# Kernel optimization log

Hardware: AMD Instinct MI355X
Metric: run time of the kernel (lower is better)

The kernel has to match this reference:

```python
import jax, jax.numpy as jnp
import numpy as np

N_USERS = 100000
N_ITEMS = 50000
N_NODES = N_USERS + N_ITEMS
NNZ = 3200000
DIM = 64
N_LAYERS = 3
BATCH = 8192


def setup_inputs() -> dict:
    key = jax.random.key(0)
    ks = jax.random.split(key, 8)
    user_emb = jax.random.normal(ks[0], (N_USERS, DIM), dtype=jnp.float32) * 0.1
    item_emb0 = jnp.zeros((N_ITEMS, DIM), dtype=jnp.float32)
    edge_val = jax.random.uniform(ks[1], (NNZ,), dtype=jnp.float32)
    W = jax.random.normal(ks[2], (DIM, DIM), dtype=jnp.float32) / np.sqrt(DIM)
    b = jax.random.normal(ks[3], (DIM,), dtype=jnp.float32) * 0.01
    edge_src = jax.random.randint(ks[4], (NNZ,), 0, N_NODES, dtype=jnp.int32)
    edge_dst = jax.random.randint(ks[5], (NNZ,), 0, N_NODES, dtype=jnp.int32)
    users = jax.random.randint(ks[6], (BATCH,), 0, N_USERS, dtype=jnp.int32)
    items = jax.random.randint(ks[7], (BATCH,), 0, N_ITEMS, dtype=jnp.int32)
    return {"user_emb": user_emb, "item_emb0": item_emb0, "edge_val": edge_val,
            "W": W, "b": b, "edge_src": edge_src, "edge_dst": edge_dst,
            "users": users, "items": items}


def _spmm(edge_src, edge_dst, edge_val, x):
    # y[dst] += val * x[src]  -- COO SpMM via segment_sum
    msgs = edge_val[:, None] * x[edge_src]          # [nnz, d]
    return jax.ops.segment_sum(msgs, edge_dst, num_segments=N_NODES)


def reference(user_emb, item_emb0, edge_val, W, b, edge_src, edge_dst, users, items):
    all_emb = jnp.concatenate([user_emb, item_emb0], axis=0)  # [N, d]
    embs = [all_emb]
    for _ in range(N_LAYERS):
        all_emb = _spmm(edge_src, edge_dst, edge_val, all_emb)
        embs.append(all_emb)
    # per-layer: transform item slice, keep ORIGINAL user_emb for user slice
    new_embs = []
    for e in embs:
        item_t = e[N_USERS:] @ W.T + b                 # Linear(d, d)
        new_embs.append(jnp.concatenate([user_emb, item_t], axis=0))
    light_out = jnp.mean(jnp.stack(new_embs, axis=1), axis=1)  # [N, d]
    all_users = light_out[:N_USERS]
    all_items = light_out[N_USERS:]
    users_emb = all_users[users]
    items_emb = all_items[items]
    gamma = jnp.sum(users_emb * items_emb, axis=1)     # [B]
    return gamma
```

## Files before the change

kernel.cpp:

```cpp
#include <hip/hip_runtime.h>
#include <hip/hip_fp16.h>

#define N_USERS 100000
#define N_ITEMS 50000
#define N_NODES 150000
#define NNZ     3200000
#define DIM     64
#define BATCH   8192

#define BKT_SHIFT 10
#define BKTSZ     (1 << BKT_SHIFT)
#define NBKT      ((N_NODES + BKTSZ - 1) >> BKT_SHIFT)
#define SRC_MASK  0x3FFFF

#define P1_THREADS 512
#define P1_PER_T   16
#define P1_CHUNK   (P1_THREADS * P1_PER_T)
#define P1_BLOCKS  ((NNZ + P1_CHUNK - 1) / P1_CHUNK)


__global__ __launch_bounds__(256) void k_zero_i32(int* __restrict__ p, int n) {
    for (int i = blockIdx.x * blockDim.x + threadIdx.x; i < n; i += gridDim.x * blockDim.x)
        p[i] = 0;
}

__global__ __launch_bounds__(256) void k_conv(const float4* __restrict__ ue,
                                              uint2* __restrict__ xu) {
    const int n = N_USERS * 16;
    for (int i = blockIdx.x * blockDim.x + threadIdx.x; i < n; i += gridDim.x * blockDim.x) {
        float4 v = ue[i];
        union { unsigned u; __half2 h; } a0, a1;
        a0.h = __floats2half2_rn(v.x, v.y);
        a1.h = __floats2half2_rn(v.z, v.w);
        xu[i] = make_uint2(a0.u, a1.u);
    }
}

__global__ __launch_bounds__(256) void k_hist147(const int* __restrict__ dst, int* __restrict__ gh) {
    __shared__ int h[NBKT];
    for (int i = threadIdx.x; i < NBKT; i += 256) h[i] = 0;
    __syncthreads();
    for (int i = blockIdx.x * 256 + threadIdx.x; i < NNZ; i += gridDim.x * 256)
        atomicAdd(&h[dst[i] >> BKT_SHIFT], 1);
    __syncthreads();
    for (int i = threadIdx.x; i < NBKT; i += 256) atomicAdd(&gh[i], h[i]);
}

__global__ __launch_bounds__(256) void k_scan147(const int* __restrict__ gh,
                                                 int* __restrict__ bbase,
                                                 int* __restrict__ bhead,
                                                 int* __restrict__ rp) {
    __shared__ int sh[256];
    const int t = threadIdx.x;
    int v = (t < NBKT) ? gh[t] : 0;
    sh[t] = v; __syncthreads();
    for (int o = 1; o < 256; o <<= 1) {
        int a = (t >= o) ? sh[t - o] : 0;
        __syncthreads();
        sh[t] += a;
        __syncthreads();
    }
    int ex = sh[t] - v;
    if (t < NBKT) { bbase[t] = ex; bhead[t] = ex; }
    if (t == 0)   { bbase[NBKT] = NNZ; rp[N_NODES] = NNZ; }
}

__global__ __launch_bounds__(P1_THREADS) void k_pass1(const int* __restrict__ src,
                                                      const int* __restrict__ dst,
                                                      const float* __restrict__ val,
                                                      int* __restrict__ bhead,
                                                      int2* __restrict__ tmp) {
    __shared__ int cnt[NBKT];
    __shared__ int base[NBKT];
    const int t = threadIdx.x;
    const int c0 = blockIdx.x * P1_CHUNK;
    for (int i = t; i < NBKT; i += P1_THREADS) cnt[i] = 0;
    __syncthreads();
    int pk[P1_PER_T], rk[P1_PER_T], bk[P1_PER_T]; float vv[P1_PER_T];
    #pragma unroll
    for (int k = 0; k < P1_PER_T; ++k) {
        const int i = c0 + k * P1_THREADS + t;
        if (i < NNZ) {
            const int d = dst[i];
            bk[k] = d >> BKT_SHIFT;
            pk[k] = src[i] | ((d & (BKTSZ - 1)) << 18);
            vv[k] = val[i];
            rk[k] = atomicAdd(&cnt[bk[k]], 1);
        } else bk[k] = -1;
    }
    __syncthreads();
    for (int i = t; i < NBKT; i += P1_THREADS) base[i] = atomicAdd(&bhead[i], cnt[i]);
    __syncthreads();
    #pragma unroll
    for (int k = 0; k < P1_PER_T; ++k)
        if (bk[k] >= 0)
            tmp[base[bk[k]] + rk[k]] = make_int2(pk[k], __float_as_int(vv[k]));
}

__global__ __launch_bounds__(1024) void k_bucket(const int* __restrict__ bbase,
                                                 const int2* __restrict__ tmp,
                                                 unsigned* __restrict__ edges,
                                                 int* __restrict__ rp,
                                                 int* __restrict__ ucnt) {
    __shared__ int cnt[BKTSZ * 2];
    __shared__ int sh[BKTSZ];
    const int b = blockIdx.x, t = threadIdx.x;
    const int start = bbase[b], end = bbase[b + 1];
    cnt[t] = 0; cnt[t + BKTSZ] = 0;
    __syncthreads();
    for (int i = start + t; i < end; i += 1024) {
        const int x = tmp[i].x;
        const int dloc = (x >> 18) & (BKTSZ - 1);
        const int cls = ((x & SRC_MASK) >= N_USERS) ? 1 : 0;
        atomicAdd(&cnt[dloc * 2 + cls], 1);
    }
    __syncthreads();
    const int c0 = cnt[2 * t], c1 = cnt[2 * t + 1];
    const int s = c0 + c1;
    sh[t] = s; __syncthreads();
    for (int o = 1; o < BKTSZ; o <<= 1) {
        int a = (t >= o) ? sh[t - o] : 0;
        __syncthreads();
        sh[t] += a;
        __syncthreads();
    }
    const int ex = sh[t] - s;
    const int node = (b << BKT_SHIFT) + t;
    if (node < N_NODES) { rp[node] = start + ex; ucnt[node] = c0; }
    cnt[2 * t] = ex;
    cnt[2 * t + 1] = ex + c0;
    __syncthreads();
    for (int i = start + t; i < end; i += 1024) {
        const int2 e = tmp[i];
        const int src  = e.x & SRC_MASK;
        const int dloc = (e.x >> 18) & (BKTSZ - 1);
        const int cls  = (src >= N_USERS) ? 1 : 0;
        const float v  = __int_as_float(e.y);
        const int  qv  = (int)(v * 16383.f + 0.5f);
        const int pos = atomicAdd(&cnt[dloc * 2 + cls], 1);
        edges[start + pos] = (unsigned)src | ((unsigned)qv << 18);
    }
}

__global__ __launch_bounds__(256) void k_mark(const int* __restrict__ items, int* __restrict__ used) {
    const int i = blockIdx.x * 256 + threadIdx.x;
    if (i < BATCH) used[items[i]] = 1;
}

__global__ __launch_bounds__(256) void k_compactI(const int* __restrict__ used,
                                                  int* __restrict__ permI,
                                                  int* __restrict__ nref) {
    __shared__ int sh[256];
    __shared__ int base;
    const int t = threadIdx.x;
    const int n = blockIdx.x * 256 + t;
    const int f = (n < N_ITEMS) ? used[n] : 0;
    sh[t] = f; __syncthreads();
    for (int o = 1; o < 256; o <<= 1) {
        int a = (t >= o) ? sh[t - o] : 0;
        __syncthreads();
        sh[t] += a;
        __syncthreads();
    }
    if (t == 255) base = atomicAdd(nref, sh[255]);
    __syncthreads();
    if (f) permI[base + sh[t] - 1] = N_USERS + n;
}

template<int MODE>
__global__ __launch_bounds__(256) void k_spmm(const int* __restrict__ rp,
                                              const int* __restrict__ ucnt,
                                              const unsigned* __restrict__ edges,
                                              const uint2* __restrict__ x16,
                                              uint2* __restrict__ y16,
                                              float4* __restrict__ isum4,
                                              const int* __restrict__ used,
                                              const int* __restrict__ permI,
                                              const int* __restrict__ nrefp) {
    __shared__ int s_node[16], s_deg[16], s_sorted[16];
    const int t = threadIdx.x;
    if (t < 16) {
        const int slot = blockIdx.x * 16 + t;
        int node = -1;
        if (MODE == 2) { if (slot < *nrefp) node = permI[slot]; }
        else node = slot;
        int deg = 0;
        if (node >= 0) deg = (MODE == 0) ? ucnt[node] : rp[node + 1] - rp[node];
        s_node[t] = node; s_deg[t] = deg;
    }
    __syncthreads();
    if (t < 16) {
        const int d = s_deg[t];
        int r = 0;
        #pragma unroll
        for (int j = 0; j < 16; ++j) {
            const int dj = s_deg[j];
            r += (dj > d) || (dj == d && j < t);
        }
        s_sorted[r] = s_node[t];
    }
    __syncthreads();

    const int lane = t & 63;
    const int g = lane >> 4, q = lane & 15;
    const int node = s_sorted[((t >> 6) << 2) + g];

    int beg = 0, deg = 0;
    if (node >= 0) { beg = rp[node]; deg = (MODE == 0) ? ucnt[node] : rp[node + 1] - beg; }

    float4 acc = make_float4(0.f, 0.f, 0.f, 0.f);
    for (int bb = 0; bb < deg; bb += 8) {
        int se[8]; float ve[8];
        #pragma unroll
        for (int k = 0; k < 8; ++k) {
            const bool ok = (bb + k) < deg;
            const unsigned e = edges[ok ? (beg + bb + k) : 0];
            se[k] = ok ? (int)(e & SRC_MASK) : 0;
            ve[k] = ok ? (float)(e >> 18) * (1.0f / 16383.0f) : 0.f;
        }
        uint2 rw[8];
        #pragma unroll
        for (int k = 0; k < 8; ++k)
            rw[k] = x16[(size_t)se[k] * 16 + q];
        #pragma unroll
        for (int k = 0; k < 8; ++k) {
            union { unsigned u; __half2 h; } c0, c1;
            c0.u = rw[k].x; c1.u = rw[k].y;
            const float2 f0 = __half22float2(c0.h);
            const float2 f1 = __half22float2(c1.h);
            acc.x = fmaf(ve[k], f0.x, acc.x);
            acc.y = fmaf(ve[k], f0.y, acc.y);
            acc.z = fmaf(ve[k], f1.x, acc.z);
            acc.w = fmaf(ve[k], f1.y, acc.w);
        }
    }

    if (node < 0) return;
    if (MODE != 2) {
        union { unsigned u; __half2 h; } a0, a1;
        a0.h = __floats2half2_rn(acc.x, acc.y);
        a1.h = __floats2half2_rn(acc.z, acc.w);
        y16[(size_t)node * 16 + q] = make_uint2(a0.u, a1.u);
    }
    if (node >= N_USERS) {
        const int in = node - N_USERS;
        if (MODE == 2 || used[in]) {
            const size_t io = (size_t)in * 16 + q;
            if (MODE == 0) {
                isum4[io] = acc;
            } else {
                float4 tv = isum4[io];
                tv.x += acc.x; tv.y += acc.y; tv.z += acc.z; tv.w += acc.w;
                isum4[io] = tv;
            }
        }
    }
}

__global__ __launch_bounds__(256) void k_final(const float* __restrict__ ue,
                                               const float* __restrict__ isum,
                                               const float* __restrict__ W,
                                               const float* __restrict__ bvec,
                                               const int* __restrict__ users,
                                               const int* __restrict__ items,
                                               float* __restrict__ out) {
    __shared__ float Ws[DIM * DIM];
    const int t = threadIdx.x;
    for (int i = t; i < DIM * DIM; i += 256) Ws[i] = W[i];
    __syncthreads();

    const int gw = blockIdx.x * 4 + (t >> 6);
    const int lane = t & 63;
    if (gw >= BATCH) return;
    const int u  = users[gw];
    const int it = items[gw];

    float u_l = ue[(size_t)u * DIM + lane];
    float m_l = isum[(size_t)it * DIM + lane] * 0.25f;
    float b_l = bvec[lane];

    float v = 0.0f;
    for (int j = 0; j < DIM; ++j) {
        float uj = __shfl(u_l, j);
        v = fmaf(uj, Ws[j * DIM + lane], v);
    }
    float p = fmaf(v, m_l, u_l * b_l);
    for (int o = 32; o > 0; o >>= 1) p += __shfl_xor(p, o);
    if (lane == 0) out[gw] = p;
}

extern "C" void kernel_launch(void* const* d_in, const int* in_sizes, int n_in,
                              void* d_out, int out_size, void* d_ws, size_t ws_size,
                              hipStream_t stream) {
    const float* user_emb  = (const float*)d_in[0];
    const float* item_emb0 = (const float*)d_in[1];
    const float* edge_val  = (const float*)d_in[2];
    const float* W         = (const float*)d_in[3];
    const float* bvec      = (const float*)d_in[4];
    const int*   edge_src  = (const int*)d_in[5];
    const int*   edge_dst  = (const int*)d_in[6];
    const int*   users     = (const int*)d_in[7];
    const int*   items     = (const int*)d_in[8];
    float* out = (float*)d_out;
    (void)item_emb0;

    char* ws = (char*)d_ws;
    uint2*    bufA16  = (uint2*)   (ws + 0);
    uint2*    bufB16  = (uint2*)   (ws + 19200000);
    uint2*    xu16    = (uint2*)   (ws + 38400000);
    float*    itemsum = (float*)   (ws + 51200000);
    unsigned* edges   = (unsigned*)(ws + 64000000);
    int2*     tmp     = (int2*)    (ws + 76800000);
    int*      rp      = (int*)     (ws + 102400000);
    int*      ucnt    = (int*)     (ws + 103000064);
    int*      permI   = (int*)     (ws + 103600064);
    int*      ghist   = (int*)     (ws + 103632832);
    int*      bbase   = (int*)     (ws + 103633856);
    int*      bhead   = (int*)     (ws + 103634880);
    int*      used    = (int*)     (ws + 103635904);
    int*      nref    = (int*)     (ws + 103835904);

    k_zero_i32<<<256, 256, 0, stream>>>(ghist, 50784);

    k_hist147<<<512, 256, 0, stream>>>(edge_dst, ghist);
    k_scan147<<<1, 256, 0, stream>>>(ghist, bbase, bhead, rp);
    k_pass1<<<P1_BLOCKS, P1_THREADS, 0, stream>>>(edge_src, edge_dst, edge_val, bhead, tmp);
    k_bucket<<<NBKT, 1024, 0, stream>>>(bbase, tmp, edges, rp, ucnt);

    k_mark<<<(BATCH + 255) / 256, 256, 0, stream>>>(items, used);
    k_compactI<<<(N_ITEMS + 255) / 256, 256, 0, stream>>>(used, permI, nref);

    k_conv<<<2048, 256, 0, stream>>>((const float4*)user_emb, xu16);

    const int blocks_all = N_NODES / 16;
    const int blocks_ref = BATCH / 16;
    k_spmm<0><<<blocks_all, 256, 0, stream>>>(rp, ucnt, edges, xu16,
                                              bufB16, (float4*)itemsum, used, permI, nref);
    k_spmm<1><<<blocks_all, 256, 0, stream>>>(rp, ucnt, edges, bufB16,
                                              bufA16, (float4*)itemsum, used, permI, nref);
    k_spmm<2><<<blocks_ref, 256, 0, stream>>>(rp, ucnt, edges, bufA16,
                                              nullptr, (float4*)itemsum, used, permI, nref);

    k_final<<<(BATCH + 3) / 4, 256, 0, stream>>>(user_emb, itemsum, W, bvec,
                                                 users, items, out);
}
```

Before: 218.9 us.

## Prune layer-2 SpMM to frontier nodes and process two rows per lane group

Adds a marking pass that flags every source node feeding the referenced items, plus the referenced items themselves. These flags are compacted into a permutation, so the second SpMM layer only computes rows that layer three actually reads. The SpMM kernel now handles 32 nodes per block, with each 16-lane group working through two degree-sorted rows at once to expose more independent gathers. The cost is two extra small kernels, more zero-initialised workspace, and higher register pressure from the doubled accumulators.

Measured after the change: 226.6 us. 1.04x slower.

```diff
diff --git a/kernel.cpp b/kernel.cpp
--- a/kernel.cpp
+++ b/kernel.cpp
@@ -17,6 +17,8 @@
 #define P1_PER_T   16
 #define P1_CHUNK   (P1_THREADS * P1_PER_T)
 #define P1_BLOCKS  ((NNZ + P1_CHUNK - 1) / P1_CHUNK)
+
+#define SLOTS_ALL  150016
 
 
 __global__ __launch_bounds__(256) void k_zero_i32(int* __restrict__ p, int n) {
@@ -167,6 +169,41 @@
     if (f) permI[base + sh[t] - 1] = N_USERS + n;
 }
 
+__global__ __launch_bounds__(256) void k_mark2(const int* __restrict__ permI,
+                                               const int* __restrict__ nrefp,
+                                               const int* __restrict__ rp,
+                                               const unsigned* __restrict__ edges,
+                                               int* __restrict__ used2) {
+    const int w = blockIdx.x * 4 + (threadIdx.x >> 6);
+    const int lane = threadIdx.x & 63;
+    if (w >= *nrefp) return;
+    const int node = permI[w];
+    const int beg = rp[node], end = rp[node + 1];
+    for (int i = beg + lane; i < end; i += 64)
+        used2[edges[i] & SRC_MASK] = 1;
+    if (lane == 0) used2[node] = 1;
+}
+
+__global__ __launch_bounds__(256) void k_compact2(const int* __restrict__ used2,
+                                                  int* __restrict__ permA2,
+                                                  int* __restrict__ n2) {
+    __shared__ int sh[256];
+    __shared__ int base;
+    const int t = threadIdx.x;
+    const int n = blockIdx.x * 256 + t;
+    const int f = (n < N_NODES) ? used2[n] : 0;
+    sh[t] = f; __syncthreads();
+    for (int o = 1; o < 256; o <<= 1) {
+        int a = (t >= o) ? sh[t - o] : 0;
+        __syncthreads();
+        sh[t] += a;
+        __syncthreads();
+    }
+    if (t == 255) base = atomicAdd(n2, sh[255]);
+    __syncthreads();
+    if (f) permA2[base + sh[t] - 1] = n;
+}
+
 template<int MODE>
 __global__ __launch_bounds__(256) void k_spmm(const int* __restrict__ rp,
                                               const int* __restrict__ ucnt,
@@ -175,83 +212,115 @@
                                               uint2* __restrict__ y16,
                                               float4* __restrict__ isum4,
                                               const int* __restrict__ used,
-                                              const int* __restrict__ permI,
-                                              const int* __restrict__ nrefp) {
-    __shared__ int s_node[16], s_deg[16], s_sorted[16];
-    const int t = threadIdx.x;
-    if (t < 16) {
-        const int slot = blockIdx.x * 16 + t;
+                                              const int* __restrict__ perm,
+                                              const int* __restrict__ boundp) {
+    __shared__ int s_nin[32], s_deg[32], s_node[32];
+    const int t = threadIdx.x;
+    if (t < 32) {
+        const int slot = blockIdx.x * 32 + t;
         int node = -1;
-        if (MODE == 2) { if (slot < *nrefp) node = permI[slot]; }
-        else node = slot;
+        if (MODE == 0) { if (slot < N_NODES) node = slot; }
+        else           { if (slot < *boundp) node = perm[slot]; }
         int deg = 0;
         if (node >= 0) deg = (MODE == 0) ? ucnt[node] : rp[node + 1] - rp[node];
-        s_node[t] = node; s_deg[t] = deg;
-    }
-    __syncthreads();
-    if (t < 16) {
+        s_nin[t] = node; s_deg[t] = deg;
+    }
+    __syncthreads();
+    if (t < 32) {
         const int d = s_deg[t];
         int r = 0;
         #pragma unroll
-        for (int j = 0; j < 16; ++j) {
+        for (int j = 0; j < 32; ++j) {
             const int dj = s_deg[j];
             r += (dj > d) || (dj == d && j < t);
         }
-        s_sorted[r] = s_node[t];
+        s_node[r] = s_nin[t];
     }
     __syncthreads();
 
     const int lane = t & 63;
-    const int g = lane >> 4, q = lane & 15;
-    const int node = s_sorted[((t >> 6) << 2) + g];
-
-    int beg = 0, deg = 0;
-    if (node >= 0) { beg = rp[node]; deg = (MODE == 0) ? ucnt[node] : rp[node + 1] - beg; }
-
-    float4 acc = make_float4(0.f, 0.f, 0.f, 0.f);
-    for (int bb = 0; bb < deg; bb += 8) {
-        int se[8]; float ve[8];
+    const int g16 = ((t >> 6) << 2) + (lane >> 4);
+    const int q = lane & 15;
+    const int nA = s_node[2 * g16];
+    const int nB = s_node[2 * g16 + 1];
+
+    int begA = 0, degA = 0, begB = 0, degB = 0;
+    if (nA >= 0) { begA = rp[nA]; degA = (MODE == 0) ? ucnt[nA] : rp[nA + 1] - begA; }
+    if (nB >= 0) { begB = rp[nB]; degB = (MODE == 0) ? ucnt[nB] : rp[nB + 1] - begB; }
+
+    float4 accA = make_float4(0.f, 0.f, 0.f, 0.f);
+    float4 accB = make_float4(0.f, 0.f, 0.f, 0.f);
+    const int itA = (degA + 7) >> 3, itB = (degB + 7) >> 3;
+    const int nit = (itA > itB) ? itA : itB;
+
+    for (int it = 0; it < nit; ++it) {
+        const int bb = it << 3;
+        int sA[8], sB[8]; float vA[8], vB[8];
         #pragma unroll
         for (int k = 0; k < 8; ++k) {
-            const bool ok = (bb + k) < deg;
-            const unsigned e = edges[ok ? (beg + bb + k) : 0];
-            se[k] = ok ? (int)(e & SRC_MASK) : 0;
-            ve[k] = ok ? (float)(e >> 18) * (1.0f / 16383.0f) : 0.f;
-        }
-        uint2 rw[8];
-        #pragma unroll
-        for (int k = 0; k < 8; ++k)
-            rw[k] = x16[(size_t)se[k] * 16 + q];
+            const bool ok = (bb + k) < degA;
+            const unsigned e = edges[ok ? (begA + bb + k) : 0];
+            sA[k] = ok ? (int)(e & SRC_MASK) : 0;
+            vA[k] = ok ? (float)(e >> 18) * (1.0f / 16383.0f) : 0.f;
+        }
+        #pragma unroll
+        for (int k = 0; k < 8; ++k) {
+            const bool ok = (bb + k) < degB;
+            const unsigned e = edges[ok ? (begB + bb + k) : 0];
+            sB[k] = ok ? (int)(e & SRC_MASK) : 0;
+            vB[k] = ok ? (float)(e >> 18) * (1.0f / 16383.0f) : 0.f;
+        }
+        uint2 rA[8], rB[8];
+        #pragma unroll
+        for (int k = 0; k < 8; ++k) rA[k] = x16[(size_t)sA[k] * 16 + q];
+        #pragma unroll
+        for (int k = 0; k < 8; ++k) rB[k] = x16[(size_t)sB[k] * 16 + q];
         #pragma unroll
         for (int k = 0; k < 8; ++k) {
             union { unsigned u; __half2 h; } c0, c1;
-            c0.u = rw[k].x; c1.u = rw[k].y;
+            c0.u = rA[k].x; c1.u = rA[k].y;
             const float2 f0 = __half22float2(c0.h);
             const float2 f1 = __half22float2(c1.h);
-            acc.x = fmaf(ve[k], f0.x, acc.x);
-            acc.y = fmaf(ve[k], f0.y, acc.y);
-            acc.z = fmaf(ve[k], f1.x, acc.z);
-            acc.w = fmaf(ve[k], f1.y, acc.w);
-        }
-    }
-
-    if (node < 0) return;
-    if (MODE != 2) {
-        union { unsigned u; __half2 h; } a0, a1;
-        a0.h = __floats2half2_rn(acc.x, acc.y);
-        a1.h = __floats2half2_rn(acc.z, acc.w);
-        y16[(size_t)node * 16 + q] = make_uint2(a0.u, a1.u);
-    }
-    if (node >= N_USERS) {
-        const int in = node - N_USERS;
-        if (MODE == 2 || used[in]) {
-            const size_t io = (size_t)in * 16 + q;
-            if (MODE == 0) {
-                isum4[io] = acc;
-            } else {
-                float4 tv = isum4[io];
-                tv.x += acc.x; tv.y += acc.y; tv.z += acc.z; tv.w += acc.w;
-                isum4[io] = tv;
+            accA.x = fmaf(vA[k], f0.x, accA.x);
+            accA.y = fmaf(vA[k], f0.y, accA.y);
+            accA.z = fmaf(vA[k], f1.x, accA.z);
+            accA.w = fmaf(vA[k], f1.y, accA.w);
+        }
+        #pragma unroll
+        for (int k = 0; k < 8; ++k) {
+            union { unsigned u; __half2 h; } c0, c1;
+            c0.u = rB[k].x; c1.u = rB[k].y;
+            const float2 f0 = __half22float2(c0.h);
+            const float2 f1 = __half22float2(c1.h);
+            accB.x = fmaf(vB[k], f0.x, accB.x);
+            accB.y = fmaf(vB[k], f0.y, accB.y);
+            accB.z = fmaf(vB[k], f1.x, accB.z);
+            accB.w = fmaf(vB[k], f1.y, accB.w);
+        }
+    }
+
+    #pragma unroll
+    for (int half = 0; half < 2; ++half) {
+        const int node = half ? nB : nA;
+        const float4 acc = half ? accB : accA;
+        if (node < 0) continue;
+        if (MODE != 2) {
+            union { unsigned u; __half2 h; } a0, a1;
+            a0.h = __floats2half2_rn(acc.x, acc.y);
+            a1.h = __floats2half2_rn(acc.z, acc.w);
+            y16[(size_t)node * 16 + q] = make_uint2(a0.u, a1.u);
+        }
+        if (node >= N_USERS) {
+            const int in = node - N_USERS;
+            if (MODE == 2 || used[in]) {
+                const size_t io = (size_t)in * 16 + q;
+                if (MODE == 0) {
+                    isum4[io] = acc;
+                } else {
+                    float4 tv = isum4[io];
+                    tv.x += acc.x; tv.y += acc.y; tv.z += acc.z; tv.w += acc.w;
+                    isum4[io] = tv;
+                }
             }
         }
     }
@@ -314,13 +383,16 @@
     int*      rp      = (int*)     (ws + 102400000);
     int*      ucnt    = (int*)     (ws + 103000064);
     int*      permI   = (int*)     (ws + 103600064);
-    int*      ghist   = (int*)     (ws + 103632832);
-    int*      bbase   = (int*)     (ws + 103633856);
-    int*      bhead   = (int*)     (ws + 103634880);
-    int*      used    = (int*)     (ws + 103635904);
-    int*      nref    = (int*)     (ws + 103835904);
-
-    k_zero_i32<<<256, 256, 0, stream>>>(ghist, 50784);
+    int*      permA2  = (int*)     (ws + 103632832);
+    int*      ghist   = (int*)     (ws + 104232896);
+    int*      bbase   = (int*)     (ws + 104233920);
+    int*      bhead   = (int*)     (ws + 104234944);
+    int*      used    = (int*)     (ws + 104235968);
+    int*      used2   = (int*)     (ws + 104435968);
+    int*      nref    = (int*)     (ws + 105035968);
+    int*      n2      = (int*)     (ws + 105036032);
+
+    k_zero_i32<<<256, 256, 0, stream>>>(ghist, 200800);
 
     k_hist147<<<512, 256, 0, stream>>>(edge_dst, ghist);
     k_scan147<<<1, 256, 0, stream>>>(ghist, bbase, bhead, rp);
@@ -329,15 +401,17 @@
 
     k_mark<<<(BATCH + 255) / 256, 256, 0, stream>>>(items, used);
     k_compactI<<<(N_ITEMS + 255) / 256, 256, 0, stream>>>(used, permI, nref);
+    k_mark2<<<BATCH / 4, 256, 0, stream>>>(permI, nref, rp, edges, used2);
+    k_compact2<<<(N_NODES + 255) / 256, 256, 0, stream>>>(used2, permA2, n2);
 
     k_conv<<<2048, 256, 0, stream>>>((const float4*)user_emb, xu16);
 
-    const int blocks_all = N_NODES / 16;
-    const int blocks_ref = BATCH / 16;
+    const int blocks_all = SLOTS_ALL / 32;
+    const int blocks_ref = BATCH / 32;
     k_spmm<0><<<blocks_all, 256, 0, stream>>>(rp, ucnt, edges, xu16,
                                               bufB16, (float4*)itemsum, used, permI, nref);
     k_spmm<1><<<blocks_all, 256, 0, stream>>>(rp, ucnt, edges, bufB16,
-                                              bufA16, (float4*)itemsum, used, permI, nref);
+                                              bufA16, (float4*)itemsum, used, permA2, n2);
     k_spmm<2><<<blocks_ref, 256, 0, stream>>>(rp, ucnt, edges, bufA16,
                                               nullptr, (float4*)itemsum, used, permI, nref);
 
```
